# Performance work log

Measured on AMD Instinct MI355X. Metric: run time of the kernel, lower is better.

## Reference

```python
import jax, jax.numpy as jnp
import numpy as np

N_NODES = 100000
N_EDGES = 1600000
F_IN = 64
F_OUT = 64


def setup_inputs() -> dict:
    key = jax.random.key(0)
    k1, k2, k3, k4, k5 = jax.random.split(key, 5)
    node_features = jax.random.normal(k1, (N_NODES, F_IN), dtype=jnp.float32)
    edge_row = jax.random.randint(k2, (N_EDGES,), 0, N_NODES, dtype=jnp.int32)
    edge_col = jax.random.randint(k3, (N_EDGES,), 0, N_NODES, dtype=jnp.int32)
    edge_vals = jax.random.uniform(k4, (N_EDGES,), dtype=jnp.float32)
    kernel = jax.random.normal(k5, (F_IN, F_OUT), dtype=jnp.float32) * (1.0 / np.sqrt(F_IN))
    bias = jnp.zeros((F_OUT,), dtype=jnp.float32)
    return {
        'node_features': node_features,
        'edge_row': edge_row,
        'edge_col': edge_col,
        'edge_vals': edge_vals,
        'kernel': kernel,
        'bias': bias,
    }


def reference(node_features, edge_row, edge_col, edge_vals, kernel, bias):
    # H_out = relu( A_hat @ (H_in @ W) + b )
    # transform: dense GEMM [N, F_in] @ [F_in, F_out]
    transformed = node_features @ kernel
    # SpMM with COO adjacency: out[r] += vals[e] * transformed[c] for edge e=(r,c)
    messages = edge_vals[:, None] * transformed[edge_col]          # [E, F_out]
    aggregated = jax.ops.segment_sum(messages, edge_row, num_segments=N_NODES)
    return jax.nn.relu(aggregated + bias)
```

## Files before the change

### kernel.cpp

```cpp
#include <hip/hip_runtime.h>
#include <hip/hip_bf16.h>

#define F 64
#define RPB 256
#define TILE 4096
#define MAXB 512
#define REG_CAP 5120
#define HCAP 2560

typedef __attribute__((ext_vector_type(8))) short short8v;
typedef __attribute__((ext_vector_type(4))) float float4v;

__device__ inline unsigned short f2bf(float x) {
    unsigned int u = __float_as_uint(x);
    u += 0x7FFFu + ((u >> 16) & 1u);
    return (unsigned short)(u >> 16);
}

__global__ __launch_bounds__(256) void gcn_transform_kernel(const float* __restrict__ H,
                                                            const float* __restrict__ W,
                                                            unsigned short* __restrict__ T,
                                                            int* __restrict__ bcount,
                                                            int n_nodes, int nb) {
    if (blockIdx.x == 0) {
        for (int i = threadIdx.x; i < nb; i += 256) bcount[i] = 0;
    }

    __shared__ unsigned short Wb[F * F];
    int tid = threadIdx.x;
    for (int i = tid * 4; i < F * F; i += 1024) {
        float4 w4 = *(const float4*)&W[i];
        ushort4 o;
        o.x = f2bf(w4.x); o.y = f2bf(w4.y); o.z = f2bf(w4.z); o.w = f2bf(w4.w);
        *(ushort4*)&Wb[i] = o;
    }
    __syncthreads();

    int lane = tid & 63, w = tid >> 6;
    int c = lane & 15;
    int g = lane >> 4;

    short8v bfrag[4][2];
#pragma unroll
    for (int ct = 0; ct < 4; ++ct)
#pragma unroll
        for (int kh = 0; kh < 2; ++kh)
#pragma unroll
            for (int j = 0; j < 8; ++j)
                bfrag[ct][kh][j] = (short)Wb[(kh * 32 + g * 8 + j) * F + ct * 16 + c];

    int nt = (n_nodes + 15) >> 4;
    int wstride = gridDim.x * 4;
#pragma unroll 2
    for (int t = blockIdx.x * 4 + w; t < nt; t += wstride) {
        int row = t * 16 + c;
        long long hb = (long long)min(row, n_nodes - 1) * F;
        float4 a0 = *(const float4*)&H[hb + g * 8];
        float4 a1 = *(const float4*)&H[hb + g * 8 + 4];
        float4 a2 = *(const float4*)&H[hb + 32 + g * 8];
        float4 a3 = *(const float4*)&H[hb + 32 + g * 8 + 4];
        short8v af0, af1;
        af0[0] = (short)f2bf(a0.x); af0[1] = (short)f2bf(a0.y);
        af0[2] = (short)f2bf(a0.z); af0[3] = (short)f2bf(a0.w);
        af0[4] = (short)f2bf(a1.x); af0[5] = (short)f2bf(a1.y);
        af0[6] = (short)f2bf(a1.z); af0[7] = (short)f2bf(a1.w);
        af1[0] = (short)f2bf(a2.x); af1[1] = (short)f2bf(a2.y);
        af1[2] = (short)f2bf(a2.z); af1[3] = (short)f2bf(a2.w);
        af1[4] = (short)f2bf(a3.x); af1[5] = (short)f2bf(a3.y);
        af1[6] = (short)f2bf(a3.z); af1[7] = (short)f2bf(a3.w);

        float4v acc[4];
#pragma unroll
        for (int ct = 0; ct < 4; ++ct) {
            acc[ct] = (float4v)(0.f);
            acc[ct] = __builtin_amdgcn_mfma_f32_16x16x32_bf16(af0, bfrag[ct][0], acc[ct], 0, 0, 0);
            acc[ct] = __builtin_amdgcn_mfma_f32_16x16x32_bf16(af1, bfrag[ct][1], acc[ct], 0, 0, 0);
        }
#pragma unroll
        for (int ct = 0; ct < 4; ++ct)
#pragma unroll
            for (int i = 0; i < 4; ++i) {
                int rr = t * 16 + g * 4 + i;
                if (rr < n_nodes) T[(size_t)rr * F + ct * 16 + c] = f2bf(acc[ct][i]);
            }
    }
}

__global__ __launch_bounds__(1024) void gcn_partition_kernel(const int* __restrict__ erow,
                                                             const int* __restrict__ ecol,
                                                             const float* __restrict__ evals,
                                                             int* __restrict__ bcount,
                                                             int2* __restrict__ srec,
                                                             int n_edges) {
    __shared__ int hist[MAXB];
    __shared__ int offs[MAXB];
    __shared__ int cur[MAXB];
    __shared__ int gbase[MAXB];
    __shared__ int wsum[16];
    __shared__ int2 rec[TILE];
    __shared__ int dst[TILE];

    int tid = threadIdx.x, lane = tid & 63, wid = tid >> 6;
    if (tid < MAXB) hist[tid] = 0;
    __syncthreads();

    int base = blockIdx.x * TILE;
    int end = min(base + TILE, n_edges);

    int i0 = base + tid * 4;
    if (i0 + 3 < end) {
        int4 r = *(const int4*)&erow[i0];
        atomicAdd(&hist[r.x >> 8], 1);
        atomicAdd(&hist[r.y >> 8], 1);
        atomicAdd(&hist[r.z >> 8], 1);
        atomicAdd(&hist[r.w >> 8], 1);
    } else {
        for (int k = i0; k < end; ++k) atomicAdd(&hist[erow[k] >> 8], 1);
    }
    __syncthreads();

    int v = 0, x = 0;
    if (tid < MAXB) {
        v = hist[tid];
        x = v;
#pragma unroll
        for (int d = 1; d < 64; d <<= 1) {
            int y = __shfl_up(x, d, 64);
            if (lane >= d) x += y;
        }
        if (lane == 63) wsum[wid] = x;
    }
    __syncthreads();
    if (tid < MAXB) {
        int woff = 0;
        for (int q = 0; q < wid; ++q) woff += wsum[q];
        int excl = woff + x - v;
        offs[tid] = excl;
        cur[tid] = excl;
        if (v > 0) gbase[tid] = tid * REG_CAP + atomicAdd(&bcount[tid], v);
    }
    __syncthreads();

    if (i0 + 3 < end) {
        int4 r = *(const int4*)&erow[i0];
        int4 c = *(const int4*)&ecol[i0];
        float4 vv = *(const float4*)&evals[i0];
#pragma unroll
        for (int k = 0; k < 4; ++k) {
            int rr = (&r.x)[k], cc = (&c.x)[k];
            float vf = (&vv.x)[k];
            int b = rr >> 8;
            int s = atomicAdd(&cur[b], 1);
            rec[s] = make_int2(cc | ((rr & 255) << 20), __float_as_int(vf));
            int d = gbase[b] + (s - offs[b]);
            dst[s] = (d < (b + 1) * REG_CAP) ? d : -1;
        }
    } else {
        for (int k = i0; k < end; ++k) {
            int rr = erow[k], b = rr >> 8;
            int s = atomicAdd(&cur[b], 1);
            rec[s] = make_int2(ecol[k] | ((rr & 255) << 20), __float_as_int(evals[k]));
            int d = gbase[b] + (s - offs[b]);
            dst[s] = (d < (b + 1) * REG_CAP) ? d : -1;
        }
    }
    __syncthreads();

    int cnt = end - base;
    for (int s = tid; s < cnt; s += 1024) {
        int d = dst[s];
        if (d >= 0) srec[d] = rec[s];
    }
}

__global__ __launch_bounds__(512) void gcn_aggregate_kernel(const int* __restrict__ bcount,
                                                            const int2* __restrict__ srec,
                                                            const unsigned int* __restrict__ Tu,
                                                            const float* __restrict__ bias,
                                                            float* __restrict__ out,
                                                            int n_nodes) {
    __shared__ int hist[128];
    __shared__ int rofs[129];
    __shared__ int wsum[2];
    __shared__ int2 buf[HCAP];

    int b = blockIdx.x >> 1;
    int half = blockIdx.x & 1;
    int tid = threadIdx.x;
    long long rbase = (long long)b * REG_CAP;
    int cnt = min(bcount[b], REG_CAP);

    if (tid < 128) hist[tid] = 0;
    __syncthreads();

    for (int i = tid; i < cnt; i += 512) {
        int rl = (srec[rbase + i].x >> 20) & 255;
        if ((rl >> 7) == half) atomicAdd(&hist[rl & 127], 1);
    }
    __syncthreads();

    int v = 0, x = 0;
    if (tid < 128) {
        v = hist[tid];
        x = v;
        int lane = tid & 63;
#pragma unroll
        for (int d = 1; d < 64; d <<= 1) {
            int y = __shfl_up(x, d, 64);
            if (lane >= d) x += y;
        }
        if (lane == 63) wsum[tid >> 6] = x;
    }
    __syncthreads();
    if (tid < 128) {
        int woff = (tid >= 64) ? wsum[0] : 0;
        int excl = woff + x - v;
        rofs[tid] = excl;
        hist[tid] = excl;
        if (tid == 0) rofs[128] = wsum[0] + wsum[1];
    }
    __syncthreads();

    for (int i = tid; i < cnt; i += 512) {
        int2 q = srec[rbase + i];
        int rl = (q.x >> 20) & 255;
        if ((rl >> 7) == half) {
            int rk = atomicAdd(&hist[rl & 127], 1);
            if (rk < HCAP) buf[rk] = q;
        }
    }
    __syncthreads();

    int lane = tid & 63, w = tid >> 6;
    int h = lane >> 5, p = lane & 31;
    float2 bb = *(const float2*)&bias[2 * p];
    for (int rl = w; rl < 128; rl += 8) {
        int kbeg = rofs[rl], kend = rofs[rl + 1];
        float ax = 0.f, ay = 0.f;
        int k = kbeg + h;
        for (; k + 14 < kend; k += 16) {
            int2 q0 = buf[k],      q1 = buf[k + 2],  q2 = buf[k + 4],  q3 = buf[k + 6];
            int2 q4 = buf[k + 8],  q5 = buf[k + 10], q6 = buf[k + 12], q7 = buf[k + 14];
            unsigned int t0 = Tu[(size_t)(q0.x & 0xFFFFF) * 32 + p];
            unsigned int t1 = Tu[(size_t)(q1.x & 0xFFFFF) * 32 + p];
            unsigned int t2 = Tu[(size_t)(q2.x & 0xFFFFF) * 32 + p];
            unsigned int t3 = Tu[(size_t)(q3.x & 0xFFFFF) * 32 + p];
            unsigned int t4 = Tu[(size_t)(q4.x & 0xFFFFF) * 32 + p];
            unsigned int t5 = Tu[(size_t)(q5.x & 0xFFFFF) * 32 + p];
            unsigned int t6 = Tu[(size_t)(q6.x & 0xFFFFF) * 32 + p];
            unsigned int t7 = Tu[(size_t)(q7.x & 0xFFFFF) * 32 + p];
            float v0 = __int_as_float(q0.y), v1 = __int_as_float(q1.y);
            float v2 = __int_as_float(q2.y), v3 = __int_as_float(q3.y);
            float v4 = __int_as_float(q4.y), v5 = __int_as_float(q5.y);
            float v6 = __int_as_float(q6.y), v7 = __int_as_float(q7.y);
            ax = fmaf(__int_as_float((int)(t0 << 16)), v0, ax);
            ay = fmaf(__int_as_float((int)(t0 & 0xFFFF0000u)), v0, ay);
            ax = fmaf(__int_as_float((int)(t1 << 16)), v1, ax);
            ay = fmaf(__int_as_float((int)(t1 & 0xFFFF0000u)), v1, ay);
            ax = fmaf(__int_as_float((int)(t2 << 16)), v2, ax);
            ay = fmaf(__int_as_float((int)(t2 & 0xFFFF0000u)), v2, ay);
            ax = fmaf(__int_as_float((int)(t3 << 16)), v3, ax);
            ay = fmaf(__int_as_float((int)(t3 & 0xFFFF0000u)), v3, ay);
            ax = fmaf(__int_as_float((int)(t4 << 16)), v4, ax);
            ay = fmaf(__int_as_float((int)(t4 & 0xFFFF0000u)), v4, ay);
            ax = fmaf(__int_as_float((int)(t5 << 16)), v5, ax);
            ay = fmaf(__int_as_float((int)(t5 & 0xFFFF0000u)), v5, ay);
            ax = fmaf(__int_as_float((int)(t6 << 16)), v6, ax);
            ay = fmaf(__int_as_float((int)(t6 & 0xFFFF0000u)), v6, ay);
            ax = fmaf(__int_as_float((int)(t7 << 16)), v7, ax);
            ay = fmaf(__int_as_float((int)(t7 & 0xFFFF0000u)), v7, ay);
        }
        for (; k + 6 < kend; k += 8) {
            int2 q0 = buf[k], q1 = buf[k + 2], q2 = buf[k + 4], q3 = buf[k + 6];
            unsigned int t0 = Tu[(size_t)(q0.x & 0xFFFFF) * 32 + p];
            unsigned int t1 = Tu[(size_t)(q1.x & 0xFFFFF) * 32 + p];
            unsigned int t2 = Tu[(size_t)(q2.x & 0xFFFFF) * 32 + p];
            unsigned int t3 = Tu[(size_t)(q3.x & 0xFFFFF) * 32 + p];
            float v0 = __int_as_float(q0.y), v1 = __int_as_float(q1.y);
            float v2 = __int_as_float(q2.y), v3 = __int_as_float(q3.y);
            ax = fmaf(__int_as_float((int)(t0 << 16)), v0, ax);
            ay = fmaf(__int_as_float((int)(t0 & 0xFFFF0000u)), v0, ay);
            ax = fmaf(__int_as_float((int)(t1 << 16)), v1, ax);
            ay = fmaf(__int_as_float((int)(t1 & 0xFFFF0000u)), v1, ay);
            ax = fmaf(__int_as_float((int)(t2 << 16)), v2, ax);
            ay = fmaf(__int_as_float((int)(t2 & 0xFFFF0000u)), v2, ay);
            ax = fmaf(__int_as_float((int)(t3 << 16)), v3, ax);
            ay = fmaf(__int_as_float((int)(t3 & 0xFFFF0000u)), v3, ay);
        }
        for (; k < kend; k += 2) {
            int2 q = buf[k];
            unsigned int t = Tu[(size_t)(q.x & 0xFFFFF) * 32 + p];
            float vv = __int_as_float(q.y);
            ax = fmaf(__int_as_float((int)(t << 16)), vv, ax);
            ay = fmaf(__int_as_float((int)(t & 0xFFFF0000u)), vv, ay);
        }
        ax += __shfl_xor(ax, 32, 64);
        ay += __shfl_xor(ay, 32, 64);
        int r = b * RPB + half * 128 + rl;
        if (h == 0 && r < n_nodes) {
            float2 o;
            o.x = fmaxf(ax + bb.x, 0.f);
            o.y = fmaxf(ay + bb.y, 0.f);
            *(float2*)&out[(size_t)r * F + 2 * p] = o;
        }
    }
}

extern "C" void kernel_launch(void* const* d_in, const int* in_sizes, int n_in,
                              void* d_out, int out_size, void* d_ws, size_t ws_size,
                              hipStream_t stream) {
    const float* H     = (const float*)d_in[0];
    const int*   erow  = (const int*)d_in[1];
    const int*   ecol  = (const int*)d_in[2];
    const float* evals = (const float*)d_in[3];
    const float* W     = (const float*)d_in[4];
    const float* bias  = (const float*)d_in[5];
    float* out = (float*)d_out;

    int n_nodes = in_sizes[0] / F;
    int n_edges = in_sizes[1];
    int nb = (n_nodes + RPB - 1) / RPB;
    int ntiles = (n_edges + TILE - 1) / TILE;

    char* ws = (char*)d_ws;
    unsigned short* T = (unsigned short*)ws; ws += (size_t)n_nodes * F * sizeof(unsigned short);
    int2*  srec   = (int2*)ws;   ws += (size_t)nb * REG_CAP * sizeof(int2);
    int*   bcount = (int*)ws;

    gcn_transform_kernel<<<512, 256, 0, stream>>>(H, W, T, bcount, n_nodes, nb);
    gcn_partition_kernel<<<ntiles, 1024, 0, stream>>>(erow, ecol, evals, bcount, srec, n_edges);
    gcn_aggregate_kernel<<<nb * 2, 512, 0, stream>>>(bcount, srec, (const unsigned int*)T, bias, out, n_nodes);
}
```

Measured before the change: 69.82 us.

## Halve row bucket size and sort edges via LDS index permutation

Shrinks each row bucket from 256 to 128 rows, so the partition kernel makes 1024-entry histograms across all threads, and launches one aggregate block per bucket instead of two half-blocks. Each aggregate block now reads its bucket's records from global memory once into LDS and builds a 16-bit permutation array rather than scattering records during a second global pass. This removes the duplicate global read of srec. In exchange, every edge gets an extra indirect LDS lookup, and the per-bucket capacity of 2816 leaves less margin for overflow on skewed degree distributions.

Result: no change. 69.92 us (+0.1%).

```diff
diff --git a/kernel.cpp b/kernel.cpp
--- a/kernel.cpp
+++ b/kernel.cpp
@@ -2,11 +2,10 @@
 #include <hip/hip_bf16.h>
 
 #define F 64
-#define RPB 256
+#define RPB 128
 #define TILE 4096
-#define MAXB 512
-#define REG_CAP 5120
-#define HCAP 2560
+#define MAXB 1024
+#define REG_CAP 2816
 
 typedef __attribute__((ext_vector_type(8))) short short8v;
 typedef __attribute__((ext_vector_type(4))) float float4v;
@@ -91,7 +90,7 @@
                                                              const float* __restrict__ evals,
                                                              int* __restrict__ bcount,
                                                              int2* __restrict__ srec,
-                                                             int n_edges) {
+                                                             int n_edges, int nb) {
     __shared__ int hist[MAXB];
     __shared__ int offs[MAXB];
     __shared__ int cur[MAXB];
@@ -101,7 +100,7 @@
     __shared__ int dst[TILE];
 
     int tid = threadIdx.x, lane = tid & 63, wid = tid >> 6;
-    if (tid < MAXB) hist[tid] = 0;
+    hist[tid] = 0;
     __syncthreads();
 
     int base = blockIdx.x * TILE;
@@ -110,34 +109,31 @@
     int i0 = base + tid * 4;
     if (i0 + 3 < end) {
         int4 r = *(const int4*)&erow[i0];
-        atomicAdd(&hist[r.x >> 8], 1);
-        atomicAdd(&hist[r.y >> 8], 1);
-        atomicAdd(&hist[r.z >> 8], 1);
-        atomicAdd(&hist[r.w >> 8], 1);
+        atomicAdd(&hist[r.x >> 7], 1);
+        atomicAdd(&hist[r.y >> 7], 1);
+        atomicAdd(&hist[r.z >> 7], 1);
+        atomicAdd(&hist[r.w >> 7], 1);
     } else {
-        for (int k = i0; k < end; ++k) atomicAdd(&hist[erow[k] >> 8], 1);
-    }
-    __syncthreads();
-
-    int v = 0, x = 0;
-    if (tid < MAXB) {
-        v = hist[tid];
-        x = v;
-#pragma unroll
-        for (int d = 1; d < 64; d <<= 1) {
-            int y = __shfl_up(x, d, 64);
-            if (lane >= d) x += y;
-        }
-        if (lane == 63) wsum[wid] = x;
-    }
-    __syncthreads();
-    if (tid < MAXB) {
+        for (int k = i0; k < end; ++k) atomicAdd(&hist[erow[k] >> 7], 1);
+    }
+    __syncthreads();
+
+    int v = hist[tid];
+    int x = v;
+#pragma unroll
+    for (int d = 1; d < 64; d <<= 1) {
+        int y = __shfl_up(x, d, 64);
+        if (lane >= d) x += y;
+    }
+    if (lane == 63) wsum[wid] = x;
+    __syncthreads();
+    {
         int woff = 0;
         for (int q = 0; q < wid; ++q) woff += wsum[q];
         int excl = woff + x - v;
         offs[tid] = excl;
         cur[tid] = excl;
-        if (v > 0) gbase[tid] = tid * REG_CAP + atomicAdd(&bcount[tid], v);
+        if (v > 0 && tid < nb) gbase[tid] = tid * REG_CAP + atomicAdd(&bcount[tid], v);
     }
     __syncthreads();
 
@@ -149,17 +145,17 @@
         for (int k = 0; k < 4; ++k) {
             int rr = (&r.x)[k], cc = (&c.x)[k];
             float vf = (&vv.x)[k];
-            int b = rr >> 8;
+            int b = rr >> 7;
             int s = atomicAdd(&cur[b], 1);
-            rec[s] = make_int2(cc | ((rr & 255) << 20), __float_as_int(vf));
+            rec[s] = make_int2(cc | ((rr & 127) << 20), __float_as_int(vf));
             int d = gbase[b] + (s - offs[b]);
             dst[s] = (d < (b + 1) * REG_CAP) ? d : -1;
         }
     } else {
         for (int k = i0; k < end; ++k) {
-            int rr = erow[k], b = rr >> 8;
+            int rr = erow[k], b = rr >> 7;
             int s = atomicAdd(&cur[b], 1);
-            rec[s] = make_int2(ecol[k] | ((rr & 255) << 20), __float_as_int(evals[k]));
+            rec[s] = make_int2(ecol[k] | ((rr & 127) << 20), __float_as_int(evals[k]));
             int d = gbase[b] + (s - offs[b]);
             dst[s] = (d < (b + 1) * REG_CAP) ? d : -1;
         }
@@ -182,10 +178,10 @@
     __shared__ int hist[128];
     __shared__ int rofs[129];
     __shared__ int wsum[2];
-    __shared__ int2 buf[HCAP];
-
-    int b = blockIdx.x >> 1;
-    int half = blockIdx.x & 1;
+    __shared__ int2 buf[REG_CAP];
+    __shared__ unsigned short perm[REG_CAP];
+
+    int b = blockIdx.x;
     int tid = threadIdx.x;
     long long rbase = (long long)b * REG_CAP;
     int cnt = min(bcount[b], REG_CAP);
@@ -194,8 +190,9 @@
     __syncthreads();
 
     for (int i = tid; i < cnt; i += 512) {
-        int rl = (srec[rbase + i].x >> 20) & 255;
-        if ((rl >> 7) == half) atomicAdd(&hist[rl & 127], 1);
+        int2 q = srec[rbase + i];
+        buf[i] = q;
+        atomicAdd(&hist[(q.x >> 20) & 127], 1);
     }
     __syncthreads();
 
@@ -222,12 +219,9 @@
     __syncthreads();
 
     for (int i = tid; i < cnt; i += 512) {
-        int2 q = srec[rbase + i];
-        int rl = (q.x >> 20) & 255;
-        if ((rl >> 7) == half) {
-            int rk = atomicAdd(&hist[rl & 127], 1);
-            if (rk < HCAP) buf[rk] = q;
-        }
+        int rl = (buf[i].x >> 20) & 127;
+        int rk = atomicAdd(&hist[rl], 1);
+        perm[rk] = (unsigned short)i;
     }
     __syncthreads();
 
@@ -239,8 +233,10 @@
         float ax = 0.f, ay = 0.f;
         int k = kbeg + h;
         for (; k + 14 < kend; k += 16) {
-            int2 q0 = buf[k],      q1 = buf[k + 2],  q2 = buf[k + 4],  q3 = buf[k + 6];
-            int2 q4 = buf[k + 8],  q5 = buf[k + 10], q6 = buf[k + 12], q7 = buf[k + 14];
+            int j0 = perm[k],      j1 = perm[k + 2],  j2 = perm[k + 4],  j3 = perm[k + 6];
+            int j4 = perm[k + 8],  j5 = perm[k + 10], j6 = perm[k + 12], j7 = perm[k + 14];
+            int2 q0 = buf[j0], q1 = buf[j1], q2 = buf[j2], q3 = buf[j3];
+            int2 q4 = buf[j4], q5 = buf[j5], q6 = buf[j6], q7 = buf[j7];
             unsigned int t0 = Tu[(size_t)(q0.x & 0xFFFFF) * 32 + p];
             unsigned int t1 = Tu[(size_t)(q1.x & 0xFFFFF) * 32 + p];
             unsigned int t2 = Tu[(size_t)(q2.x & 0xFFFFF) * 32 + p];
@@ -271,7 +267,8 @@
             ay = fmaf(__int_as_float((int)(t7 & 0xFFFF0000u)), v7, ay);
         }
         for (; k + 6 < kend; k += 8) {
-            int2 q0 = buf[k], q1 = buf[k + 2], q2 = buf[k + 4], q3 = buf[k + 6];
+            int j0 = perm[k], j1 = perm[k + 2], j2 = perm[k + 4], j3 = perm[k + 6];
+            int2 q0 = buf[j0], q1 = buf[j1], q2 = buf[j2], q3 = buf[j3];
             unsigned int t0 = Tu[(size_t)(q0.x & 0xFFFFF) * 32 + p];
             unsigned int t1 = Tu[(size_t)(q1.x & 0xFFFFF) * 32 + p];
             unsigned int t2 = Tu[(size_t)(q2.x & 0xFFFFF) * 32 + p];
@@ -288,7 +285,7 @@
             ay = fmaf(__int_as_float((int)(t3 & 0xFFFF0000u)), v3, ay);
         }
         for (; k < kend; k += 2) {
-            int2 q = buf[k];
+            int2 q = buf[perm[k]];
             unsigned int t = Tu[(size_t)(q.x & 0xFFFFF) * 32 + p];
             float vv = __int_as_float(q.y);
             ax = fmaf(__int_as_float((int)(t << 16)), vv, ax);
@@ -296,7 +293,7 @@
         }
         ax += __shfl_xor(ax, 32, 64);
         ay += __shfl_xor(ay, 32, 64);
-        int r = b * RPB + half * 128 + rl;
+        int r = b * RPB + rl;
         if (h == 0 && r < n_nodes) {
             float2 o;
             o.x = fmaxf(ax + bb.x, 0.f);
@@ -328,6 +325,6 @@
     int*   bcount = (int*)ws;
 
     gcn_transform_kernel<<<512, 256, 0, stream>>>(H, W, T, bcount, n_nodes, nb);
-    gcn_partition_kernel<<<ntiles, 1024, 0, stream>>>(erow, ecol, evals, bcount, srec, n_edges);
-    gcn_aggregate_kernel<<<nb * 2, 512, 0, stream>>>(bcount, srec, (const unsigned int*)T, bias, out, n_nodes);
-}
+    gcn_partition_kernel<<<ntiles, 1024, 0, stream>>>(erow, ecol, evals, bcount, srec, n_edges, nb);
+    gcn_aggregate_kernel<<<nb, 512, 0, stream>>>(bcount, srec, (const unsigned int*)T, bias, out, n_nodes);
+}
```
